# Kernel tuning notes

Measured on AMD Instinct MI355X. Metric: run time of the kernel, lower is better.

Reference implementation:

```python
import jax, jax.numpy as jnp
import numpy as np

# Static conv config (matches init_kwargs)
STRIDE = (1, 1, 1)
PAD = (1, 1, 1)
DIL = (1, 1, 1)
DG = 1  # deformable groups


def setup_inputs() -> dict:
    key = jax.random.key(0)
    k1, k2, k3 = jax.random.split(key, 3)
    N, Cin, T, H, W = 2, 32, 8, 56, 56
    Cout, kT, kH, kW = 64, 3, 3, 3
    x = jax.random.normal(k1, (N, Cin, T, H, W), dtype=jnp.float32)
    # offset channels = DG * 3 * kT*kH*kW = 81 ; layout [N, dg*K*3, To, Ho, Wo]
    offset = jax.random.normal(k2, (N, DG * 3 * kT * kH * kW, T, H, W), dtype=jnp.float32)
    stdv = 1.0 / np.sqrt(Cin * kT * kH * kW)
    weight = jax.random.uniform(k3, (Cout, Cin, kT, kH, kW), dtype=jnp.float32, minval=-stdv, maxval=stdv)
    bias = jnp.zeros((Cout,), dtype=jnp.float32)
    return {"x": x, "offset": offset, "weight": weight, "bias": bias}


def _deform_conv3d(x, offset, weight, bias):
    N, C, T, H, W = x.shape
    Co, _, kT, kH, kW = weight.shape
    K = kT * kH * kW
    st, sh, sw = STRIDE
    pt_, ph_, pw_ = PAD
    dt_, dh_, dw_ = DIL
    To = (T + 2 * pt_ - (dt_ * (kT - 1) + 1)) // st + 1
    Ho = (H + 2 * ph_ - (dh_ * (kH - 1) + 1)) // sh + 1
    Wo = (W + 2 * pw_ - (dw_ * (kW - 1) + 1)) // sw + 1
    Cg = C // DG
    # offsets: [N, DG, K, 3(dt,dh,dw), To, Ho, Wo]
    off = offset.reshape(N, DG, K, 3, To, Ho, Wo)
    kt, kh, kw = [g.reshape(-1) for g in jnp.meshgrid(
        jnp.arange(kT), jnp.arange(kH), jnp.arange(kW), indexing='ij')]
    # base sampling grid per kernel tap: [K, To, Ho, Wo] via broadcasting
    bt = (jnp.arange(To) * st - pt_)[None, :, None, None] + (kt * dt_)[:, None, None, None]
    bh = (jnp.arange(Ho) * sh - ph_)[None, None, :, None] + (kh * dh_)[:, None, None, None]
    bw = (jnp.arange(Wo) * sw - pw_)[None, None, None, :] + (kw * dw_)[:, None, None, None]
    # fractional sampling positions: [N, DG, K, To, Ho, Wo]
    pt = bt[None, None] + off[:, :, :, 0]
    ph = bh[None, None] + off[:, :, :, 1]
    pw = bw[None, None] + off[:, :, :, 2]
    t0f, h0f, w0f = jnp.floor(pt), jnp.floor(ph), jnp.floor(pw)
    lt, lh, lw = pt - t0f, ph - h0f, pw - w0f
    t0 = t0f.astype(jnp.int32)
    h0 = h0f.astype(jnp.int32)
    w0 = w0f.astype(jnp.int32)
    x_flat = x.reshape(N, DG, Cg, T * H * W)
    acc = jnp.zeros((N, DG, Cg, K, To, Ho, Wo), dtype=x.dtype)
    for ct in (0, 1):
        ti = t0 + ct
        wt = lt if ct else (1.0 - lt)
        for ch in (0, 1):
            hi = h0 + ch
            wh = lh if ch else (1.0 - lh)
            for cw in (0, 1):
                wi = w0 + cw
                ww = lw if cw else (1.0 - lw)
                valid = ((ti >= 0) & (ti < T) & (hi >= 0) & (hi < H) & (wi >= 0) & (wi < W))
                idx = (jnp.clip(ti, 0, T - 1) * H + jnp.clip(hi, 0, H - 1)) * W + jnp.clip(wi, 0, W - 1)
                v = jnp.take_along_axis(x_flat, idx.reshape(N, DG, 1, -1), axis=3)
                v = v.reshape(N, DG, Cg, K, To, Ho, Wo)
                wgt = (wt * wh * ww * valid.astype(x.dtype))[:, :, None]  # [N,DG,1,K,To,Ho,Wo]
                acc = acc + v * wgt
    w_r = weight.reshape(Co, DG, Cg, K)
    out = jnp.einsum('ogck,ngcktuv->notuv', w_r, acc)
    if bias.size > 0:
        out = out + bias[None, :, None, None, None]
    return out


def reference(x, offset, weight, bias):
    return _deform_conv3d(x, offset, weight, bias)
```

## Files before the change

kernel.cpp:

```cpp
#include <hip/hip_runtime.h>
#include <hip/hip_fp16.h>

#define CIN   32
#define COUT  64
#define TT    8
#define HH    56
#define WW    56
#define KK    27
#define SP    (TT * HH * WW)
#define NB    2
#define POSB  32
#define NBLK  ((NB * SP) / POSB)
#define NBLKP 784

typedef __attribute__((ext_vector_type(8))) _Float16 half8;
typedef __attribute__((ext_vector_type(4))) float    f32x4;

#define WF_OFF   0
#define XTH_OFF  (128 << 10)

__global__ __launch_bounds__(256) void prep_kernel(const float* __restrict__ x,
                                                   const float* __restrict__ w,
                                                   __half* __restrict__ xTh,
                                                   __half* __restrict__ wf) {
    const int b = blockIdx.x;
    const int t = threadIdx.x;
    if (b < NBLKP) {
        __shared__ float sm[CIN][65];
        const int s0 = b * 64, n = s0 / SP, sp0 = s0 % SP;
#pragma unroll
        for (int it = 0; it < 8; ++it) {
            const int idx = it * 256 + t, c = idx >> 6, l = idx & 63;
            sm[c][l] = x[((size_t)n * CIN + c) * SP + sp0 + l];
        }
        __syncthreads();
#pragma unroll
        for (int it = 0; it < 4; ++it) {
            const int idx = it * 256 + t, l = idx >> 4, cp = idx & 15;
            ((__half2*)xTh)[((size_t)n * SP + sp0 + l) * (CIN / 2) + cp] =
                __floats2half2_rn(sm[2 * cp][l], sm[2 * cp + 1][l]);
        }
    } else {
        const int k = b - NBLKP;
#pragma unroll
        for (int it = 0; it < 8; ++it) {
            const int idx  = it * 256 + t;
            const int j    = idx & 7;
            const int lane = (idx >> 3) & 63;
            const int ct   = (idx >> 9) & 3;
            const int co   = ct * 16 + (lane & 15);
            const int c    = (lane >> 4) * 8 + j;
            wf[(((size_t)k * 4 + ct) * 64 + lane) * 8 + j] =
                __float2half(w[((size_t)co * CIN + c) * KK + k]);
        }
    }
}

__global__ __launch_bounds__(512, 8) void dconv3d_kernel(const __half* __restrict__ xTh,
                                                         const float* __restrict__ off,
                                                         const __half* __restrict__ wf,
                                                         const float* __restrict__ bias,
                                                         float* __restrict__ out) {
    __shared__ __align__(16) char smem[3 * 16 * 2 * 64 * 4];
    float (*offs)[POSB] = reinterpret_cast<float(*)[POSB]>(smem);
    float (*cmb)[16][2][64] = reinterpret_cast<float(*)[16][2][64]>(smem);

    const int t    = threadIdx.x;
    const int lane = t & 63;
    const int wv   = t >> 6;
    const int wpos = wv & 1;
    const int q    = wv >> 1;

    const int posI = lane >> 2;
    const int cgI  = lane & 3;
    const int jg   = lane >> 4;

    const int bp_addr = (((lane & 15) << 2) | jg) << 2;

    const int sb  = (blockIdx.x & 7) * 196 + (blockIdx.x >> 3);
    const int s0  = sb * POSB;
    const int n   = s0 / SP;
    const int spb = s0 % SP;

    {
        const float* offbase = off + ((size_t)n * (3 * KK)) * SP + spb;
        for (int i = t; i < 81 * 8; i += 512) {
            const int row = i >> 3, qd = i & 7;
            *(float4*)&offs[row][qd * 4] = *(const float4*)(offbase + (size_t)row * SP + qd * 4);
        }
    }
    __syncthreads();

    const int pl = wpos * 16 + posI;
    const int sp = spb + pl;
    const int to = sp / (HH * WW);
    const int hw = sp % (HH * WW);
    const int ho = hw / WW;
    const int wo = hw % WW;

    f32x4 acc[4];
#pragma unroll
    for (int ct = 0; ct < 4; ++ct)
#pragma unroll
        for (int r = 0; r < 4; ++r)
            acc[ct][r] = q ? 0.f : bias[ct * 16 + jg * 4 + r];

    const __half* xn = xTh + (size_t)n * SP * CIN;

    const int kbeg = q * 7;
    const int kend = (q == 3) ? KK : kbeg + 7;

    for (int k = kbeg; k < kend; ++k) {
        const int kt  = k / 9;
        const int khh = (k / 3) % 3;
        const int kww = k % 3;

        const float pt_ = (float)(to - 1 + kt)  + offs[k * 3 + 0][pl];
        const float ph_ = (float)(ho - 1 + khh) + offs[k * 3 + 1][pl];
        const float pw_ = (float)(wo - 1 + kww) + offs[k * 3 + 2][pl];

        const float ft = floorf(pt_), fh = floorf(ph_), fw = floorf(pw_);
        const float lt = pt_ - ft, lh = ph_ - fh, lw = pw_ - fw;
        const int t0 = (int)ft, h0 = (int)fh, w0 = (int)fw;
        const int t1 = t0 + 1, h1 = h0 + 1, w1 = w0 + 1;

        float awt[2], awh[2], aww[2];
        int   it2[2], ih2[2], iw2[2];
        awt[0] = (t0 >= 0 && t0 < TT) ? (1.f - lt) : 0.f;
        awt[1] = (t1 >= 0 && t1 < TT) ? lt : 0.f;
        it2[0] = min(max(t0, 0), TT - 1);  it2[1] = min(max(t1, 0), TT - 1);
        awh[0] = (h0 >= 0 && h0 < HH) ? (1.f - lh) : 0.f;
        awh[1] = (h1 >= 0 && h1 < HH) ? lh : 0.f;
        ih2[0] = min(max(h0, 0), HH - 1);  ih2[1] = min(max(h1, 0), HH - 1);
        aww[0] = (w0 >= 0 && w0 < WW) ? (1.f - lw) : 0.f;
        aww[1] = (w1 >= 0 && w1 < WW) ? lw : 0.f;
        iw2[0] = min(max(w0, 0), WW - 1);  iw2[1] = min(max(w1, 0), WW - 1);

        int   a[8];
        float cw[8];
#pragma unroll
        for (int ci = 0; ci < 8; ++ci) {
            const int i0 = ci >> 2, i1 = (ci >> 1) & 1, i2 = ci & 1;
            a[ci]  = (it2[i0] * HH + ih2[i1]) * WW + iw2[i2];
            cw[ci] = awt[i0] * awh[i1] * aww[i2];
        }

        float4 g[8];
#pragma unroll
        for (int ci = 0; ci < 8; ++ci)
            g[ci] = *(const float4*)(xn + (size_t)a[ci] * CIN + cgI * 8);

        __half2 vacc[4];
#pragma unroll
        for (int j = 0; j < 4; ++j) vacc[j] = __floats2half2_rn(0.f, 0.f);
#pragma unroll
        for (int ci = 0; ci < 8; ++ci) {
            const __half2* uh = (const __half2*)&g[ci];
            const __half2 cw2 = __float2half2_rn(cw[ci]);
            vacc[0] = __hfma2(cw2, uh[0], vacc[0]);
            vacc[1] = __hfma2(cw2, uh[1], vacc[1]);
            vacc[2] = __hfma2(cw2, uh[2], vacc[2]);
            vacc[3] = __hfma2(cw2, uh[3], vacc[3]);
        }

        union { __half2 h2[4]; int i[4]; half8 h8; } u, v;
#pragma unroll
        for (int d = 0; d < 4; ++d) u.h2[d] = vacc[d];
#pragma unroll
        for (int d = 0; d < 4; ++d)
            v.i[d] = __builtin_amdgcn_ds_bpermute(bp_addr, u.i[d]);
        const half8 bfrag = v.h8;

#pragma unroll
        for (int ct = 0; ct < 4; ++ct) {
            const half8 af = *(const half8*)(wf + (((size_t)k * 4 + ct) * 64 + lane) * 8);
            acc[ct] = __builtin_amdgcn_mfma_f32_16x16x32_f16(af, bfrag, acc[ct], 0, 0, 0);
        }
    }

    __syncthreads();
    if (q != 0) {
#pragma unroll
        for (int ct = 0; ct < 4; ++ct)
#pragma unroll
            for (int r = 0; r < 4; ++r)
                cmb[q - 1][ct * 4 + r][wpos][lane] = acc[ct][r];
    }
    __syncthreads();
    if (q == 0) {
#pragma unroll
        for (int ct = 0; ct < 4; ++ct)
#pragma unroll
            for (int r = 0; r < 4; ++r) {
                const int co = ct * 16 + jg * 4 + r;
                float v = acc[ct][r];
#pragma unroll
                for (int j = 0; j < 3; ++j) v += cmb[j][ct * 4 + r][wpos][lane];
                out[((size_t)n * COUT + co) * SP + spb + wpos * 16 + (lane & 15)] = v;
            }
    }
}

extern "C" void kernel_launch(void* const* d_in, const int* in_sizes, int n_in,
                              void* d_out, int out_size, void* d_ws, size_t ws_size,
                              hipStream_t stream) {
    const float* x    = (const float*)d_in[0];
    const float* off  = (const float*)d_in[1];
    const float* w    = (const float*)d_in[2];
    const float* bias = (const float*)d_in[3];
    float* out        = (float*)d_out;

    __half* wf  = (__half*)((char*)d_ws + WF_OFF);
    __half* xTh = (__half*)((char*)d_ws + XTH_OFF);

    prep_kernel<<<NBLKP + KK, 256, 0, stream>>>(x, w, xTh, wf);
    dconv3d_kernel<<<NBLK, 512, 0, stream>>>(xTh, off, wf, bias, out);
}
```

Baseline: 125.7 us.

## Tile positions as 8x4 spatial patches and stage a halo slab of x in LDS

Each block now covers an 8x4 spatial tile (instead of 32 linear positions) and preloads an 8x18x14 voxel halo slab of the fp16 channels-last input into shared memory. The bilinear gathers then read from LDS when every sample in the wavefront falls inside the slab, with a wave-uniform fallback to global loads otherwise. This aims to replace scattered global/L2 gathers with LDS reads, at the cost of about 140KB of LDS per block, lower occupancy (launch bounds 512,2), and an extra slab fill per block.

```diff
diff --git a/kernel.cpp b/kernel.cpp
--- a/kernel.cpp
+++ b/kernel.cpp
@@ -13,6 +13,13 @@
 #define NBLK  ((NB * SP) / POSB)
 #define NBLKP 784
 
+#define SH    18
+#define SW    14
+#define SLABVOX (8 * SH * SW)
+#define OFFS_B  (81 * POSB * 4)
+#define SLAB_B  (SLABVOX * 64)
+#define SMEM_B  (OFFS_B + SLAB_B)
+
 typedef __attribute__((ext_vector_type(8))) _Float16 half8;
 typedef __attribute__((ext_vector_type(4))) float    f32x4;
 
@@ -56,14 +63,15 @@
     }
 }
 
-__global__ __launch_bounds__(512, 8) void dconv3d_kernel(const __half* __restrict__ xTh,
+__global__ __launch_bounds__(512, 2) void dconv3d_kernel(const __half* __restrict__ xTh,
                                                          const float* __restrict__ off,
                                                          const __half* __restrict__ wf,
                                                          const float* __restrict__ bias,
                                                          float* __restrict__ out) {
-    __shared__ __align__(16) char smem[3 * 16 * 2 * 64 * 4];
-    float (*offs)[POSB] = reinterpret_cast<float(*)[POSB]>(smem);
-    float (*cmb)[16][2][64] = reinterpret_cast<float(*)[16][2][64]>(smem);
+    __shared__ __align__(16) char smem[SMEM_B];
+    float*  offs  = reinterpret_cast<float*>(smem);
+    __half* slabh = reinterpret_cast<__half*>(smem + OFFS_B);
+    float (*cmb)[16][2][64] = reinterpret_cast<float(*)[16][2][64]>(smem + OFFS_B);
 
     const int t    = threadIdx.x;
     const int lane = t & 63;
@@ -77,35 +85,56 @@
 
     const int bp_addr = (((lane & 15) << 2) | jg) << 2;
 
-    const int sb  = (blockIdx.x & 7) * 196 + (blockIdx.x >> 3);
-    const int s0  = sb * POSB;
-    const int n   = s0 / SP;
-    const int spb = s0 % SP;
+    const int sb = (blockIdx.x & 7) * 196 + (blockIdx.x >> 3);
+    const int n  = sb / 784;
+    const int r  = sb % 784;
+    const int to = r / 98;
+    const int rr = r % 98;
+    const int hp = rr / 14;
+    const int wp = rr % 14;
+    const int h_lo = hp * 8 - 5;
+    const int w_lo = wp * 4 - 5;
+
+    const __half* xn = xTh + (size_t)n * SP * CIN;
 
     {
-        const float* offbase = off + ((size_t)n * (3 * KK)) * SP + spb;
-        for (int i = t; i < 81 * 8; i += 512) {
-            const int row = i >> 3, qd = i & 7;
-            *(float4*)&offs[row][qd * 4] = *(const float4*)(offbase + (size_t)row * SP + qd * 4);
+        const float* ob = off + (size_t)n * 81 * SP + ((size_t)to * HH) * WW + wp * 4;
+        for (int u = t; u < 81 * 8; u += 512) {
+            const int r81 = u >> 3, hr = u & 7;
+            *(float4*)&offs[r81 * POSB + hr * 4] =
+                *(const float4*)(ob + (size_t)r81 * SP + (hp * 8 + hr) * WW);
+        }
+    }
+    {
+        for (int u = t; u < SLABVOX * 4; u += 512) {
+            const int q16 = u & 3;
+            const int vox = u >> 2;
+            const int sw  = vox % SW;
+            const int t2  = vox / SW;
+            const int sh  = t2 % SH;
+            const int tt  = t2 / SH;
+            const int gh  = h_lo + sh;
+            const int gw  = w_lo + sw;
+            if ((unsigned)gh < HH && (unsigned)gw < WW) {
+                *(float4*)(slabh + (size_t)vox * 32 + q16 * 8) =
+                    *(const float4*)(xn + ((size_t)(tt * HH + gh) * WW + gw) * CIN + q16 * 8);
+            }
         }
     }
     __syncthreads();
 
-    const int pl = wpos * 16 + posI;
-    const int sp = spb + pl;
-    const int to = sp / (HH * WW);
-    const int hw = sp % (HH * WW);
-    const int ho = hw / WW;
-    const int wo = hw % WW;
+    const int prow = wpos * 4 + (posI >> 2);
+    const int pcol = posI & 3;
+    const int pl   = wpos * 16 + posI;
+    const int ho   = hp * 8 + prow;
+    const int wo   = wp * 4 + pcol;
 
     f32x4 acc[4];
 #pragma unroll
     for (int ct = 0; ct < 4; ++ct)
 #pragma unroll
-        for (int r = 0; r < 4; ++r)
-            acc[ct][r] = q ? 0.f : bias[ct * 16 + jg * 4 + r];
-
-    const __half* xn = xTh + (size_t)n * SP * CIN;
+        for (int r2 = 0; r2 < 4; ++r2)
+            acc[ct][r2] = q ? 0.f : bias[ct * 16 + jg * 4 + r2];
 
     const int kbeg = q * 7;
     const int kend = (q == 3) ? KK : kbeg + 7;
@@ -115,9 +144,9 @@
         const int khh = (k / 3) % 3;
         const int kww = k % 3;
 
-        const float pt_ = (float)(to - 1 + kt)  + offs[k * 3 + 0][pl];
-        const float ph_ = (float)(ho - 1 + khh) + offs[k * 3 + 1][pl];
-        const float pw_ = (float)(wo - 1 + kww) + offs[k * 3 + 2][pl];
+        const float pt_ = (float)(to - 1 + kt)  + offs[(k * 3 + 0) * POSB + pl];
+        const float ph_ = (float)(ho - 1 + khh) + offs[(k * 3 + 1) * POSB + pl];
+        const float pw_ = (float)(wo - 1 + kww) + offs[(k * 3 + 2) * POSB + pl];
 
         const float ft = floorf(pt_), fh = floorf(ph_), fw = floorf(pw_);
         const float lt = pt_ - ft, lh = ph_ - fh, lw = pw_ - fw;
@@ -136,19 +165,35 @@
         aww[1] = (w1 >= 0 && w1 < WW) ? lw : 0.f;
         iw2[0] = min(max(w0, 0), WW - 1);  iw2[1] = min(max(w1, 0), WW - 1);
 
-        int   a[8];
+        int sh2[2], sw2[2];
+        sh2[0] = ih2[0] - h_lo;  sh2[1] = ih2[1] - h_lo;
+        sw2[0] = iw2[0] - w_lo;  sw2[1] = iw2[1] - w_lo;
+        const int oos = !((unsigned)sh2[0] < SH && (unsigned)sh2[1] < SH &&
+                          (unsigned)sw2[0] < SW && (unsigned)sw2[1] < SW);
+
         float cw[8];
 #pragma unroll
         for (int ci = 0; ci < 8; ++ci) {
             const int i0 = ci >> 2, i1 = (ci >> 1) & 1, i2 = ci & 1;
-            a[ci]  = (it2[i0] * HH + ih2[i1]) * WW + iw2[i2];
             cw[ci] = awt[i0] * awh[i1] * aww[i2];
         }
 
         float4 g[8];
-#pragma unroll
-        for (int ci = 0; ci < 8; ++ci)
-            g[ci] = *(const float4*)(xn + (size_t)a[ci] * CIN + cgI * 8);
+        if (__builtin_expect(__any(oos), 0)) {
+#pragma unroll
+            for (int ci = 0; ci < 8; ++ci) {
+                const int i0 = ci >> 2, i1 = (ci >> 1) & 1, i2 = ci & 1;
+                const int a = (it2[i0] * HH + ih2[i1]) * WW + iw2[i2];
+                g[ci] = *(const float4*)(xn + (size_t)a * CIN + cgI * 8);
+            }
+        } else {
+#pragma unroll
+            for (int ci = 0; ci < 8; ++ci) {
+                const int i0 = ci >> 2, i1 = (ci >> 1) & 1, i2 = ci & 1;
+                const int vox = (it2[i0] * SH + sh2[i1]) * SW + sw2[i2];
+                g[ci] = *(const float4*)(slabh + (size_t)vox * 32 + cgI * 8);
+            }
+        }
 
         __half2 vacc[4];
 #pragma unroll
@@ -163,13 +208,13 @@
             vacc[3] = __hfma2(cw2, uh[3], vacc[3]);
         }
 
-        union { __half2 h2[4]; int i[4]; half8 h8; } u, v;
-#pragma unroll
-        for (int d = 0; d < 4; ++d) u.h2[d] = vacc[d];
+        union { __half2 h2[4]; int i[4]; half8 h8; } u2, v2;
+#pragma unroll
+        for (int d = 0; d < 4; ++d) u2.h2[d] = vacc[d];
 #pragma unroll
         for (int d = 0; d < 4; ++d)
-            v.i[d] = __builtin_amdgcn_ds_bpermute(bp_addr, u.i[d]);
-        const half8 bfrag = v.h8;
+            v2.i[d] = __builtin_amdgcn_ds_bpermute(bp_addr, u2.i[d]);
+        const half8 bfrag = v2.h8;
 
 #pragma unroll
         for (int ct = 0; ct < 4; ++ct) {
@@ -183,20 +228,24 @@
 #pragma unroll
         for (int ct = 0; ct < 4; ++ct)
 #pragma unroll
-            for (int r = 0; r < 4; ++r)
-                cmb[q - 1][ct * 4 + r][wpos][lane] = acc[ct][r];
+            for (int r2 = 0; r2 < 4; ++r2)
+                cmb[q - 1][ct * 4 + r2][wpos][lane] = acc[ct][r2];
     }
     __syncthreads();
     if (q == 0) {
+        const int posC = lane & 15;
+        const int rowC = wpos * 4 + (posC >> 2);
+        const int colC = posC & 3;
+        const int spo  = ((size_t)0, (to * HH + hp * 8 + rowC) * WW + wp * 4 + colC);
 #pragma unroll
         for (int ct = 0; ct < 4; ++ct)
 #pragma unroll
-            for (int r = 0; r < 4; ++r) {
-                const int co = ct * 16 + jg * 4 + r;
-                float v = acc[ct][r];
-#pragma unroll
-                for (int j = 0; j < 3; ++j) v += cmb[j][ct * 4 + r][wpos][lane];
-                out[((size_t)n * COUT + co) * SP + spb + wpos * 16 + (lane & 15)] = v;
+            for (int r2 = 0; r2 < 4; ++r2) {
+                const int co = ct * 16 + jg * 4 + r2;
+                float v = acc[ct][r2];
+#pragma unroll
+                for (int j = 0; j < 3; ++j) v += cmb[j][ct * 4 + r2][wpos][lane];
+                out[((size_t)n * COUT + co) * SP + spo] = v;
             }
     }
 }
```

Result: slower. 154.7 us (+23.0%).
